# Performance work log

Measured on AMD Instinct MI355X. Metric: run time of the kernel, lower is better.

The kernel has to match this reference:

```python
import jax, jax.numpy as jnp
import numpy as np
import math

MIN_NORM = 1e-15
PROJ_EPS = 4e-3  # float32 boundary eps used by HGCN PoincareBall
C = 1.0          # curvature


def _artanh(x):
    return jnp.arctanh(jnp.clip(x, -1.0 + 1e-7, 1.0 - 1e-7))


def proj(x, c):
    norm = jnp.maximum(jnp.linalg.norm(x, axis=-1, keepdims=True), MIN_NORM)
    maxnorm = (1.0 - PROJ_EPS) / jnp.sqrt(c)
    return jnp.where(norm > maxnorm, x / norm * maxnorm, x)


def lambda_x(x, c):
    x2 = jnp.sum(x * x, axis=-1, keepdims=True)
    return 2.0 / jnp.maximum(1.0 - c * x2, MIN_NORM)


def mobius_add(x, y, c):
    x2 = jnp.sum(x * x, axis=-1, keepdims=True)
    y2 = jnp.sum(y * y, axis=-1, keepdims=True)
    xy = jnp.sum(x * y, axis=-1, keepdims=True)
    num = (1.0 + 2.0 * c * xy + c * y2) * x + (1.0 - c * x2) * y
    denom = 1.0 + 2.0 * c * xy + (c ** 2) * x2 * y2
    return num / jnp.maximum(denom, MIN_NORM)


def logmap0(p, c):
    sqrt_c = jnp.sqrt(c)
    p_norm = jnp.maximum(jnp.linalg.norm(p, axis=-1, keepdims=True), MIN_NORM)
    return _artanh(sqrt_c * p_norm) * p / (p_norm * sqrt_c)


def logmap(p1, p2, c):
    # tangent vector at p1 pointing to p2
    sub = mobius_add(-p1, p2, c)
    sub_norm = jnp.maximum(jnp.linalg.norm(sub, axis=-1, keepdims=True), MIN_NORM)
    lam = lambda_x(p1, c)
    sqrt_c = jnp.sqrt(c)
    return 2.0 / (sqrt_c * lam) * _artanh(sqrt_c * sub_norm) * sub / sub_norm


def expmap(u, p, c):
    # exp map of tangent u at base point p
    sqrt_c = jnp.sqrt(c)
    u_norm = jnp.maximum(jnp.linalg.norm(u, axis=-1, keepdims=True), MIN_NORM)
    second = jnp.tanh(sqrt_c / 2.0 * lambda_x(p, c) * u_norm) * u / (sqrt_c * u_norm)
    return mobius_add(p, second, c)


def setup_inputs() -> dict:
    key = jax.random.key(0)
    k1, k2, k3 = jax.random.split(key, 3)
    N, D = 768, 128
    x = jax.random.normal(k1, (N, D), jnp.float32) * 0.1
    x = proj(x, C)  # valid points on the Poincare ball
    adj = (jax.random.uniform(k2, (N, N), jnp.float32) < 0.04).astype(jnp.float32)
    att_w = jax.random.normal(k3, (2 * D, 1), jnp.float32) * (1.0 / math.sqrt(2 * D))
    att_b = jnp.zeros((1,), jnp.float32)
    return {"x": x, "adj": adj, "att_w": att_w, "att_b": att_b}


def reference(x, adj, att_w, att_b):
    c = C
    D = x.shape[-1]
    x_tangent = logmap0(x, c)                               # [N, D]
    # pairwise logmap: tangent at x_i pointing to x_j -> [N, N, D]
    x_local_tangent = logmap(x[:, None, :], x[None, :, :], c)
    # DenseAtt: sigmoid(Linear([xt_i ; xt_j])) * adj, factorized to avoid [N,N,2D]
    s_left = x_tangent @ att_w[:D, 0]                        # [N]
    s_right = x_tangent @ att_w[D:, 0]                       # [N]
    adj_att = jax.nn.sigmoid(s_left[:, None] + s_right[None, :] + att_b[0]) * adj
    support_t = jnp.einsum('ij,ijd->id', adj_att, x_local_tangent)  # [N, D]
    output = proj(expmap(support_t, x, c), c)
    return output
```

## Files before the change

kernel.cpp:

```cpp
#include <hip/hip_runtime.h>
#include <math.h>

#define NN 768
#define DD 128
#define XC 64

__device__ __forceinline__ double wred_d64(double v) {
    #pragma unroll
    for (int o = 32; o > 0; o >>= 1) v += __shfl_down(v, o, 64);
    return v;
}

__global__ __launch_bounds__(256) void hypagg_fused(
        const float* __restrict__ x,
        const float* __restrict__ adj,
        const float* __restrict__ att_w,
        const float* __restrict__ att_b,
        float* __restrict__ out) {
    __shared__ float xi[DD];
    __shared__ float wr[DD];
    __shared__ float xcache[XC][DD];
    __shared__ int   list[NN];
    __shared__ float aval[NN];
    __shared__ float dots[NN];
    __shared__ float y2s[NN];
    __shared__ float rds[NN];
    __shared__ float bco[NN];
    __shared__ int   counter;
    __shared__ double pre[2][2];
    __shared__ double s_x2i, s_beta, s_sLi, s_b0;
    __shared__ double cpart[4];
    __shared__ double epart[2][3];

    const int i = blockIdx.x, t = threadIdx.x;
    const int wid = t >> 6, lane = t & 63;

    float xv = 0.0f;
    if (t < DD) {
        xv = x[i * DD + t];
        xi[t] = xv;
        wr[t] = att_w[DD + t];
        double dx2 = wred_d64((double)xv * xv);
        double dwl = wred_d64((double)xv * (double)att_w[t]);
        if (lane == 0) { pre[wid][0] = dx2; pre[wid][1] = dwl; }
    }
    if (t == 0) counter = 0;
    __syncthreads();

    if (t == 0) {
        double x2 = pre[0][0] + pre[1][0];
        double dl = pre[0][1] + pre[1][1];
        double r  = sqrt(x2);
        double g0 = atanh(fmin(r, 1.0 - 1e-7)) / fmax(r, 1e-15);
        s_x2i = x2;
        s_beta = 1.0 - x2;
        s_sLi = g0 * dl;
        s_b0  = (double)att_b[0];
    }

    if (t < NN / 4) {
        float4 a = ((const float4*)(adj + (size_t)i * NN))[t];
        int m = (a.x != 0.0f) + (a.y != 0.0f) + (a.z != 0.0f) + (a.w != 0.0f);
        if (m) {
            int base = atomicAdd(&counter, m);
            int j = 4 * t;
            if (a.x != 0.0f) { list[base] = j;     aval[base] = a.x; ++base; }
            if (a.y != 0.0f) { list[base] = j + 1; aval[base] = a.y; ++base; }
            if (a.z != 0.0f) { list[base] = j + 2; aval[base] = a.z; ++base; }
            if (a.w != 0.0f) { list[base] = j + 3; aval[base] = a.w; ++base; }
        }
    }
    __syncthreads();
    const int n = counter;

    {
        const int hw = t >> 5;
        const int hl = t & 31;
        const float4 xw = ((const float4*)xi)[hl];
        const float4 ww = ((const float4*)wr)[hl];
        for (int k = hw; k < n; k += 8) {
            float4 a = ((const float4*)(x + (size_t)list[k] * DD))[hl];
            if (k < XC) ((float4*)xcache[k])[hl] = a;
            double dd = (double)xw.x * a.x + (double)xw.y * a.y
                      + (double)xw.z * a.z + (double)xw.w * a.w;
            double dy = (double)a.x * a.x + (double)a.y * a.y
                      + (double)a.z * a.z + (double)a.w * a.w;
            float  dr = ww.x * a.x + ww.y * a.y + ww.z * a.z + ww.w * a.w;
            #pragma unroll
            for (int o = 16; o > 0; o >>= 1) {
                dd += __shfl_down(dd, o, 32);
                dy += __shfl_down(dy, o, 32);
                dr += __shfl_down(dr, o, 32);
            }
            if (hl == 0) { dots[k] = (float)dd; y2s[k] = (float)dy; rds[k] = dr; }
        }
    }
    __syncthreads();

    double asum = 0.0;
    {
        const double x2i = s_x2i, beta = s_beta, sLi = s_sLi, b0 = s_b0;
        const double factor = fmax(beta, 1e-15);
        for (int k = t; k < n; k += 256) {
            double dot = (double)dots[k];
            double y2  = (double)y2s[k];
            double ry  = sqrt(y2);
            double g0j = atanh(fmin(ry, 1.0 - 1e-7)) / fmax(ry, 1e-15);
            double z   = sLi + g0j * (double)rds[k] + b0;
            double w   = (double)aval[k] / (1.0 + exp(-z));
            double alpha  = 1.0 - 2.0 * dot + y2;
            double denomc = fmax(1.0 - 2.0 * dot + x2i * y2, 1e-15);
            double sn2 = (alpha * alpha * x2i - 2.0 * alpha * beta * dot + beta * beta * y2)
                         / (denomc * denomc);
            double sn  = fmax(sqrt(fmax(sn2, 0.0)), 1e-15);
            double g   = atanh(fmin(sn, 1.0 - 1e-7)) / sn;
            double common = w * factor * g / denomc;
            asum -= common * alpha;
            bco[k] = (float)(common * beta);
        }
    }
    asum = wred_d64(asum);
    if (lane == 0) cpart[wid] = asum;
    __syncthreads();

    double u = 0.0;
    if (t < DD) {
        const double rowA = cpart[0] + cpart[1] + cpart[2] + cpart[3];
        u = rowA * (double)xv;
        const int nc = (n < XC) ? n : XC;
        for (int k = 0; k < nc; ++k)
            u += (double)bco[k] * (double)xcache[k][t];
        for (int k = XC; k < n; ++k)
            u += (double)bco[k] * (double)x[(size_t)list[k] * DD + t];
        double p_un2 = wred_d64(u * u);
        double p_xu  = wred_d64((double)xv * u);
        if (lane == 0) { epart[wid][0] = p_un2; epart[wid][1] = p_xu; }
    }
    __syncthreads();

    double ov = 0.0;
    if (t < DD) {
        double un2 = epart[0][0] + epart[1][0];
        double xu  = epart[0][1] + epart[1][1];
        double lamfac = fmax(s_beta, 1e-15);
        double un = fmax(sqrt(un2), 1e-15);
        double th = tanh(un / lamfac);
        double s  = th / un;
        double y2 = s * s * un2;
        double xy = s * xu;
        double c1 = 1.0 + 2.0 * xy + y2;
        double c2 = 1.0 - s_x2i;
        double den = fmax(1.0 + 2.0 * xy + s_x2i * y2, 1e-15);
        ov = (c1 * (double)xv + c2 * s * u) / den;
        double p_on2 = wred_d64(ov * ov);
        if (lane == 0) epart[wid][2] = p_on2;
    }
    __syncthreads();

    if (t < DD) {
        double on2 = epart[0][2] + epart[1][2];
        double on  = fmax(sqrt(on2), 1e-15);
        const double maxn = 1.0 - 4e-3;
        double scale = (on > maxn) ? (maxn / on) : 1.0;
        out[i * DD + t] = (float)(ov * scale);
    }
}

extern "C" void kernel_launch(void* const* d_in, const int* in_sizes, int n_in,
                              void* d_out, int out_size, void* d_ws, size_t ws_size,
                              hipStream_t stream) {
    const float* x     = (const float*)d_in[0];
    const float* adj   = (const float*)d_in[1];
    const float* att_w = (const float*)d_in[2];
    const float* att_b = (const float*)d_in[3];
    float* out = (float*)d_out;
    hypagg_fused<<<NN, 256, 0, stream>>>(x, adj, att_w, att_b, out);
}
```

Baseline: 71.84 us.

## Precompute per-row norms and attention scores in a separate prologue kernel

```diff
diff --git a/kernel.cpp b/kernel.cpp
--- a/kernel.cpp
+++ b/kernel.cpp
@@ -5,30 +5,45 @@
 #define DD 128
 #define XC 64
 
-__device__ __forceinline__ double wred_d64(double v) {
+__global__ __launch_bounds__(64) void row_kernel(
+        const float* __restrict__ x, const float* __restrict__ att_w,
+        double* __restrict__ x2a, double* __restrict__ sL, double* __restrict__ sR) {
+    const int i = blockIdx.x, lane = threadIdx.x;
+    const float2 xv = ((const float2*)(x + (size_t)i * DD))[lane];
+    const float2 wl = ((const float2*)att_w)[lane];
+    const float2 wr = ((const float2*)(att_w + DD))[lane];
+    double dx2 = (double)xv.x * xv.x + (double)xv.y * xv.y;
+    double dl  = (double)xv.x * wl.x + (double)xv.y * wl.y;
+    double dr  = (double)xv.x * wr.x + (double)xv.y * wr.y;
     #pragma unroll
-    for (int o = 32; o > 0; o >>= 1) v += __shfl_down(v, o, 64);
-    return v;
+    for (int o = 32; o > 0; o >>= 1) {
+        dx2 += __shfl_down(dx2, o, 64);
+        dl  += __shfl_down(dl,  o, 64);
+        dr  += __shfl_down(dr,  o, 64);
+    }
+    if (lane == 0) {
+        double r  = sqrt(dx2);
+        double g0 = atanh(fmin(r, 1.0 - 1e-7)) / fmax(r, 1e-15);
+        x2a[i] = dx2;
+        sL[i]  = g0 * dl;
+        sR[i]  = g0 * dr;
+    }
 }
 
-__global__ __launch_bounds__(256) void hypagg_fused(
-        const float* __restrict__ x,
-        const float* __restrict__ adj,
-        const float* __restrict__ att_w,
+__global__ __launch_bounds__(256) void hypagg_main(
+        const float* __restrict__ x, const float* __restrict__ adj,
         const float* __restrict__ att_b,
-        float* __restrict__ out) {
-    __shared__ float xi[DD];
-    __shared__ float wr[DD];
-    __shared__ float xcache[XC][DD];
-    __shared__ int   list[NN];
-    __shared__ float aval[NN];
-    __shared__ float dots[NN];
-    __shared__ float y2s[NN];
-    __shared__ float rds[NN];
-    __shared__ float bco[NN];
-    __shared__ int   counter;
-    __shared__ double pre[2][2];
-    __shared__ double s_x2i, s_beta, s_sLi, s_b0;
+        const double* __restrict__ x2a, const double* __restrict__ sL,
+        const double* __restrict__ sR, float* __restrict__ out) {
+    __shared__ float  xi[DD];
+    __shared__ float  xcache[XC][DD];
+    __shared__ int    list[NN];
+    __shared__ float  aval[NN];
+    __shared__ double dots[NN];
+    __shared__ float  bco[NN];
+    __shared__ double upart[DD];
+    __shared__ int    counter;
+    __shared__ double s_x2i, s_sLi, s_b0;
     __shared__ double cpart[4];
     __shared__ double epart[2][3];
 
@@ -36,27 +51,14 @@
     const int wid = t >> 6, lane = t & 63;
 
     float xv = 0.0f;
-    if (t < DD) {
-        xv = x[i * DD + t];
-        xi[t] = xv;
-        wr[t] = att_w[DD + t];
-        double dx2 = wred_d64((double)xv * xv);
-        double dwl = wred_d64((double)xv * (double)att_w[t]);
-        if (lane == 0) { pre[wid][0] = dx2; pre[wid][1] = dwl; }
-    }
-    if (t == 0) counter = 0;
-    __syncthreads();
-
+    if (t < DD) { xv = x[i * DD + t]; xi[t] = xv; }
     if (t == 0) {
-        double x2 = pre[0][0] + pre[1][0];
-        double dl = pre[0][1] + pre[1][1];
-        double r  = sqrt(x2);
-        double g0 = atanh(fmin(r, 1.0 - 1e-7)) / fmax(r, 1e-15);
-        s_x2i = x2;
-        s_beta = 1.0 - x2;
-        s_sLi = g0 * dl;
+        counter = 0;
+        s_x2i = x2a[i];
+        s_sLi = sL[i];
         s_b0  = (double)att_b[0];
     }
+    __syncthreads();
 
     if (t < NN / 4) {
         float4 a = ((const float4*)(adj + (size_t)i * NN))[t];
@@ -74,39 +76,39 @@
     const int n = counter;
 
     {
-        const int hw = t >> 5;
-        const int hl = t & 31;
-        const float4 xw = ((const float4*)xi)[hl];
-        const float4 ww = ((const float4*)wr)[hl];
-        for (int k = hw; k < n; k += 8) {
-            float4 a = ((const float4*)(x + (size_t)list[k] * DD))[hl];
-            if (k < XC) ((float4*)xcache[k])[hl] = a;
-            double dd = (double)xw.x * a.x + (double)xw.y * a.y
-                      + (double)xw.z * a.z + (double)xw.w * a.w;
-            double dy = (double)a.x * a.x + (double)a.y * a.y
-                      + (double)a.z * a.z + (double)a.w * a.w;
-            float  dr = ww.x * a.x + ww.y * a.y + ww.z * a.z + ww.w * a.w;
+        const int g  = t >> 4;
+        const int gl = t & 15;
+        const float4 xa = ((const float4*)xi)[gl];
+        const float4 xb = ((const float4*)xi)[16 + gl];
+        for (int k = g; k < n; k += 16) {
+            const float4* xj4 = (const float4*)(x + (size_t)list[k] * DD);
+            float4 a = xj4[gl];
+            float4 b = xj4[16 + gl];
+            if (k < XC) {
+                ((float4*)xcache[k])[gl]      = a;
+                ((float4*)xcache[k])[16 + gl] = b;
+            }
+            double dd = (double)xa.x * a.x + (double)xa.y * a.y
+                      + (double)xa.z * a.z + (double)xa.w * a.w
+                      + (double)xb.x * b.x + (double)xb.y * b.y
+                      + (double)xb.z * b.z + (double)xb.w * b.w;
             #pragma unroll
-            for (int o = 16; o > 0; o >>= 1) {
-                dd += __shfl_down(dd, o, 32);
-                dy += __shfl_down(dy, o, 32);
-                dr += __shfl_down(dr, o, 32);
-            }
-            if (hl == 0) { dots[k] = (float)dd; y2s[k] = (float)dy; rds[k] = dr; }
+            for (int o = 8; o > 0; o >>= 1) dd += __shfl_down(dd, o, 16);
+            if (gl == 0) dots[k] = dd;
         }
     }
     __syncthreads();
 
     double asum = 0.0;
     {
-        const double x2i = s_x2i, beta = s_beta, sLi = s_sLi, b0 = s_b0;
+        const double x2i = s_x2i, sLi = s_sLi, b0 = s_b0;
+        const double beta = 1.0 - x2i;
         const double factor = fmax(beta, 1e-15);
         for (int k = t; k < n; k += 256) {
-            double dot = (double)dots[k];
-            double y2  = (double)y2s[k];
-            double ry  = sqrt(y2);
-            double g0j = atanh(fmin(ry, 1.0 - 1e-7)) / fmax(ry, 1e-15);
-            double z   = sLi + g0j * (double)rds[k] + b0;
+            const int j = list[k];
+            double dot = dots[k];
+            double y2  = x2a[j];
+            double z   = sLi + sR[j] + b0;
             double w   = (double)aval[k] / (1.0 + exp(-z));
             double alpha  = 1.0 - 2.0 * dot + y2;
             double denomc = fmax(1.0 - 2.0 * dot + x2i * y2, 1e-15);
@@ -119,40 +121,55 @@
             bco[k] = (float)(common * beta);
         }
     }
-    asum = wred_d64(asum);
+    #pragma unroll
+    for (int o = 32; o > 0; o >>= 1) asum += __shfl_down(asum, o, 64);
     if (lane == 0) cpart[wid] = asum;
     __syncthreads();
 
-    double u = 0.0;
-    if (t < DD) {
-        const double rowA = cpart[0] + cpart[1] + cpart[2] + cpart[3];
-        u = rowA * (double)xv;
+    {
+        const int d = t & (DD - 1);
+        const int h = t >> 7;
+        double p = 0.0;
         const int nc = (n < XC) ? n : XC;
-        for (int k = 0; k < nc; ++k)
-            u += (double)bco[k] * (double)xcache[k][t];
-        for (int k = XC; k < n; ++k)
-            u += (double)bco[k] * (double)x[(size_t)list[k] * DD + t];
-        double p_un2 = wred_d64(u * u);
-        double p_xu  = wred_d64((double)xv * u);
-        if (lane == 0) { epart[wid][0] = p_un2; epart[wid][1] = p_xu; }
+        for (int k = h; k < nc; k += 2) p += (double)bco[k] * (double)xcache[k][d];
+        for (int k = XC + h; k < n; k += 2) p += (double)bco[k] * (double)x[(size_t)list[k] * DD + d];
+        if (h == 1) upart[d] = p;
+        __syncthreads();
+        if (t < DD) {
+            const double rowA = cpart[0] + cpart[1] + cpart[2] + cpart[3];
+            double u = rowA * (double)xv + p + upart[d];
+            double p_un2 = u * u;
+            double p_xu  = (double)xv * u;
+            #pragma unroll
+            for (int o = 32; o > 0; o >>= 1) {
+                p_un2 += __shfl_down(p_un2, o, 64);
+                p_xu  += __shfl_down(p_xu,  o, 64);
+            }
+            if (lane == 0) { epart[wid][0] = p_un2; epart[wid][1] = p_xu; }
+            upart[d] = u;
+        }
     }
     __syncthreads();
 
     double ov = 0.0;
     if (t < DD) {
+        double u   = upart[t];
         double un2 = epart[0][0] + epart[1][0];
         double xu  = epart[0][1] + epart[1][1];
-        double lamfac = fmax(s_beta, 1e-15);
+        double x2i = s_x2i;
+        double lamfac = fmax(1.0 - x2i, 1e-15);
         double un = fmax(sqrt(un2), 1e-15);
         double th = tanh(un / lamfac);
         double s  = th / un;
         double y2 = s * s * un2;
         double xy = s * xu;
         double c1 = 1.0 + 2.0 * xy + y2;
-        double c2 = 1.0 - s_x2i;
-        double den = fmax(1.0 + 2.0 * xy + s_x2i * y2, 1e-15);
+        double c2 = 1.0 - x2i;
+        double den = fmax(1.0 + 2.0 * xy + x2i * y2, 1e-15);
         ov = (c1 * (double)xv + c2 * s * u) / den;
-        double p_on2 = wred_d64(ov * ov);
+        double p_on2 = ov * ov;
+        #pragma unroll
+        for (int o = 32; o > 0; o >>= 1) p_on2 += __shfl_down(p_on2, o, 64);
         if (lane == 0) epart[wid][2] = p_on2;
     }
     __syncthreads();
@@ -174,5 +191,11 @@
     const float* att_w = (const float*)d_in[2];
     const float* att_b = (const float*)d_in[3];
     float* out = (float*)d_out;
-    hypagg_fused<<<NN, 256, 0, stream>>>(x, adj, att_w, att_b, out);
+
+    double* x2a = (double*)d_ws;
+    double* sL  = x2a + NN;
+    double* sR  = sL + NN;
+
+    row_kernel<<<NN, 64, 0, stream>>>(x, att_w, x2a, sL, sR);
+    hypagg_main<<<NN, 256, 0, stream>>>(x, adj, att_b, x2a, sL, sR, out);
 }
```

After: 71.20 us. No clear change (-0.9%).
